# Optimization experiments

Measured on AMD Instinct MI355X. Metric: run time of the kernel, lower is better.

## Reference

```python
import jax, jax.numpy as jnp
import numpy as np

B = 131072
IN_DIM = 100
H = 256


def setup_inputs() -> dict:
    key = jax.random.key(0)
    ks = jax.random.split(key, 7)
    return {
        "x": jax.random.normal(ks[0], (B, IN_DIM), dtype=jnp.float32),
        "C": jax.random.normal(ks[1], (B, H), dtype=jnp.float32),
        "h": jax.random.normal(ks[2], (B, H), dtype=jnp.float32),
        # stacked gate weights, gate order: i, f, g, o  (equivalent to 8 separate Linears)
        "Wx": jax.random.normal(ks[3], (IN_DIM, 4 * H), dtype=jnp.float32) * 0.05,
        "Wh": jax.random.normal(ks[4], (H, 4 * H), dtype=jnp.float32) * 0.05,
        "bx": jax.random.normal(ks[5], (4 * H,), dtype=jnp.float32) * 0.05,
        "bh": jax.random.normal(ks[6], (4 * H,), dtype=jnp.float32) * 0.05,
    }


def reference(x, C, h, Wx, Wh, bx, bh):
    # two fused GEMMs replace the 8 per-gate Linears (same math)
    gates = (x @ Wx + bx) + (h @ Wh + bh)  # [B, 4H]
    i_pre, f_pre, g_pre, o_pre = jnp.split(gates, 4, axis=-1)
    i = jax.nn.sigmoid(i_pre)
    f = jax.nn.sigmoid(f_pre)
    g = jnp.tanh(g_pre)
    o = jax.nn.sigmoid(o_pre)
    c_out = f * C + i * g
    h_out = o * jnp.tanh(c_out)
    return (c_out, h_out)
```

## Files before the change

### kernel.cpp

```cpp
#include <hip/hip_runtime.h>
#include <stdint.h>


typedef short bf16x8 __attribute__((ext_vector_type(8)));
typedef float f32x4  __attribute__((ext_vector_type(4)));

#define HDIM   256
#define INDIM  100
#define NROWS  131072
#define BT_OFF 0
#define XB_OFF (1048576 / 2)
#define HB_OFF (35651584 / 2)
#define ABUF(b) ((b) * 8192)
#define BBUF(b) (24576 + (b) * 16384)

__device__ __forceinline__ float fexp(float x) {
  return __builtin_amdgcn_exp2f(x * 1.44269504088896340736f);
}
__device__ __forceinline__ float frcp(float x) { return __builtin_amdgcn_rcpf(x); }
__device__ __forceinline__ float sigm(float x) { return frcp(1.0f + fexp(-x)); }
__device__ __forceinline__ float tanh_fast(float x) {
  return 1.0f - 2.0f * frcp(1.0f + fexp(2.0f * x));
}
__device__ __forceinline__ unsigned short f2bf_rne(float f) {
  union { float f; uint32_t u; } v; v.f = f;
  return (unsigned short)((v.u + 0x7FFFu + ((v.u >> 16) & 1u)) >> 16);
}
__device__ __forceinline__ void gl16(const void* g, void* l) {
  __builtin_amdgcn_global_load_lds(
      (const __attribute__((address_space(1))) unsigned int*)g,
      (__attribute__((address_space(3))) unsigned int*)l, 16, 0, 0);
}
#define VMW(N) asm volatile("s_waitcnt vmcnt(" #N ")" ::: "memory")

__global__ void prep_all(const float* __restrict__ X, const float* __restrict__ Hin,
                         const float* __restrict__ Wx, const float* __restrict__ Wh,
                         const float* __restrict__ bxp, const float* __restrict__ bhp,
                         unsigned short* __restrict__ ws) {
  const int b = blockIdx.x, tid = threadIdx.x;
  if (b < 8192) {
    const int t   = b * 256 + tid;
    const int row = t >> 4, k0 = (t & 15) * 8;
    const float* xp = X + (size_t)row * INDIM;
    float4 lo = make_float4(0.f, 0.f, 0.f, 0.f);
    float4 hi = make_float4(0.f, 0.f, 0.f, 0.f);
    if (k0 + 4 <= INDIM) lo = *reinterpret_cast<const float4*>(xp + k0);
    if (k0 + 8 <= INDIM) hi = *reinterpret_cast<const float4*>(xp + k0 + 4);
    float va[8] = {lo.x, lo.y, lo.z, lo.w, hi.x, hi.y, hi.z, hi.w};
    unsigned short o[8];
#pragma unroll
    for (int e = 0; e < 8; ++e) {
      const int k = k0 + e;
      const float f = (k < INDIM) ? va[e] : (k == 127 ? 1.0f : 0.0f);
      o[e] = f2bf_rne(f);
    }
    *reinterpret_cast<bf16x8*>(ws + XB_OFF + (size_t)row * 128 + k0) =
        *reinterpret_cast<bf16x8*>(o);
  } else if (b < 24576) {
    const int t   = (b - 8192) * 256 + tid;
    const int row = t >> 5, k0 = (t & 31) * 8;
    const float* hp = Hin + (size_t)row * HDIM + k0;
    const float4 lo = *reinterpret_cast<const float4*>(hp);
    const float4 hi = *reinterpret_cast<const float4*>(hp + 4);
    unsigned short o[8] = {f2bf_rne(lo.x), f2bf_rne(lo.y), f2bf_rne(lo.z),
                           f2bf_rne(lo.w), f2bf_rne(hi.x), f2bf_rne(hi.y),
                           f2bf_rne(hi.z), f2bf_rne(hi.w)};
    *reinterpret_cast<bf16x8*>(ws + HB_OFF + (size_t)row * 256 + k0) =
        *reinterpret_cast<bf16x8*>(o);
  } else {
    const int unit = (b - 24576) * 4 + (tid >> 6);
    const int lane = tid & 63;
    const int kst  = unit % 12;
    const int fidb = unit / 12;
    const int bn   = fidb >> 3, fid = fidb & 7;
    const int g    = fid >> 1,  wc  = fid & 1;
    const int wcol = g * HDIM + bn * 32 + wc * 16 + (lane & 15);
    const int kb   = kst * 32 + (lane >> 4) * 8;
    unsigned short v[8];
#pragma unroll
    for (int e = 0; e < 8; ++e) {
      const int k = kb + e;
      float f = 0.0f;
      if (k < INDIM)     f = Wx[(size_t)k * 1024 + wcol];
      else if (k == 127) f = bxp[wcol] + bhp[wcol];
      else if (k >= 128) f = Wh[(size_t)(k - 128) * 1024 + wcol];
      v[e] = f2bf_rne(f);
    }
    *reinterpret_cast<bf16x8*>(ws + BT_OFF + (size_t)unit * 512 + lane * 8) =
        *reinterpret_cast<bf16x8*>(v);
  }
}

__global__ __launch_bounds__(512, 2)
void lstm_main(const unsigned short* __restrict__ ws,
               const float* __restrict__ Cin, float* __restrict__ out)
{
  __shared__ unsigned char smem[73728];

  const int tid  = threadIdx.x;
  const int orig = blockIdx.x;
  const int lg   = ((orig & 7) << 9) | (orig >> 3);
  const int mt   = lg >> 2;
  const int bnn  = lg & 3;

  const int lane = tid & 63;
  const int l15  = lane & 15;
  const int kq   = lane >> 4;
  const int wid  = tid >> 6;
  const int wr   = wid >> 2;
  const int wcq  = wid & 3;
  const int ch   = bnn * 64 + wcq * 16 + l15;
  const int sx   = (l15 >> 1) & 3;

  const unsigned short* xb = ws + XB_OFF;
  const unsigned short* hb = ws + HB_OFF;
  const unsigned short* Bt = ws + BT_OFF;

  const int ci = wid * 64 + lane;
  const int r  = ci >> 2;
  const int sc = (ci & 3) ^ ((r >> 1) & 3);
  const unsigned short* xsrc = xb + (size_t)(mt * 128 + r) * 128 + sc * 8;
  const unsigned short* hsrc = hb + (size_t)(mt * 128 + r) * 256 + sc * 8;

  const unsigned short* bsrc[2];
#pragma unroll
  for (int j = 0; j < 2; ++j) {
    const int u  = wid * 2 + j;
    const int gu = (bnn * 2 + (u >> 3)) * 8 + (u & 7);
    bsrc[j] = Bt + (size_t)gu * 12 * 512 + lane * 8;
  }
  const int adst = wid * 1024;
  const int bd0  = (wid * 2 + 0) * 1024;
  const int bd1  = (wid * 2 + 1) * 1024;

  f32x4 acc[4][4];
#pragma unroll
  for (int m = 0; m < 4; ++m)
#pragma unroll
    for (int g = 0; g < 4; ++g)
#pragma unroll
      for (int e = 0; e < 4; ++e) acc[m][g][e] = 0.0f;

  float cvv[4][4];

  auto STAGE = [&](int T) {
    char* Ad = (char*)smem + ABUF(T % 3);
    char* Bd = (char*)smem + BBUF(T % 3);
    if (T < 4) gl16(xsrc + T * 32, Ad + adst);
    else       gl16(hsrc + (T - 4) * 32, Ad + adst);
    gl16(bsrc[0] + T * 512, Bd + bd0);
    gl16(bsrc[1] + T * 512, Bd + bd1);
  };

  auto COMPUTE = [&](int S) {
    const unsigned short* Ab = (const unsigned short*)(smem + ABUF(S % 3));
    const unsigned short* Bb = (const unsigned short*)(smem + BBUF(S % 3));
    bf16x8 afr[4], bfr[4];
#pragma unroll
    for (int m = 0; m < 4; ++m)
      afr[m] = *reinterpret_cast<const bf16x8*>(
          Ab + (wr * 64 + m * 16 + l15) * 32 + ((kq ^ sx) * 8));
#pragma unroll
    for (int g = 0; g < 4; ++g) {
      const int ub = (wcq >> 1) * 8 + g * 2 + (wcq & 1);
      bfr[g] = *reinterpret_cast<const bf16x8*>(Bb + ub * 512 + lane * 8);
    }
    __builtin_amdgcn_s_setprio(1);
#pragma unroll
    for (int m = 0; m < 4; ++m)
#pragma unroll
      for (int g = 0; g < 4; ++g)
        acc[m][g] = __builtin_amdgcn_mfma_f32_16x16x32_bf16(
            afr[m], bfr[g], acc[m][g], 0, 0, 0);
    __builtin_amdgcn_s_setprio(0);
  };

  STAGE(0);
  STAGE(1);

#define STEP(S, KN)                                               \
  do {                                                            \
    VMW(KN);                                                      \
    __builtin_amdgcn_s_barrier();                                 \
    if ((S) + 2 < 12) STAGE((S) + 2);                             \
    if ((S) == 9) {                                               \
      const float* cb =                                           \
          Cin + ((size_t)mt * 128 + wr * 64 + kq * 4) * HDIM + ch;\
      _Pragma("unroll")                                           \
      for (int m = 0; m < 4; ++m)                                 \
        _Pragma("unroll")                                         \
        for (int e = 0; e < 4; ++e)                               \
          cvv[m][e] = __builtin_nontemporal_load(                 \
              cb + (size_t)(m * 16 + e) * HDIM);                  \
    }                                                             \
    COMPUTE(S);                                                   \
  } while (0)

  STEP(0, 3);  STEP(1, 3);  STEP(2, 3);  STEP(3, 3);
  STEP(4, 3);  STEP(5, 3);  STEP(6, 3);  STEP(7, 3);
  STEP(8, 3);  STEP(9, 3);  STEP(10, 19); STEP(11, 16);
#undef STEP

  VMW(0);

  float* op  = out + ((size_t)mt * 128 + wr * 64 + kq * 4) * HDIM + ch;
  float* op2 = op + (size_t)NROWS * HDIM;
#pragma unroll
  for (int m = 0; m < 4; ++m) {
#pragma unroll
    for (int e = 0; e < 4; ++e) {
      const float pi = acc[m][0][e];
      const float pf = acc[m][1][e];
      const float pg = acc[m][2][e];
      const float po = acc[m][3][e];
      const float ig = sigm(pi), fg = sigm(pf);
      const float gg = tanh_fast(pg), og = sigm(po);
      const float co = fg * cvv[m][e] + ig * gg;
      const float ho = og * tanh_fast(co);
      __builtin_nontemporal_store(co, op  + (size_t)(m * 16 + e) * HDIM);
      __builtin_nontemporal_store(ho, op2 + (size_t)(m * 16 + e) * HDIM);
    }
  }
}

extern "C" void kernel_launch(void* const* d_in, const int* in_sizes, int n_in,
                              void* d_out, int out_size, void* d_ws, size_t ws_size,
                              hipStream_t stream) {
  const float* x  = (const float*)d_in[0];
  const float* C  = (const float*)d_in[1];
  const float* h  = (const float*)d_in[2];
  const float* Wx = (const float*)d_in[3];
  const float* Wh = (const float*)d_in[4];
  const float* bx = (const float*)d_in[5];
  const float* bh = (const float*)d_in[6];
  float* o = (float*)d_out;
  unsigned short* ws = (unsigned short*)d_ws;

  prep_all<<<dim3(24768), dim3(256), 0, stream>>>(x, h, Wx, Wh, bx, bh, ws);
  lstm_main<<<dim3(4096), dim3(512), 0, stream>>>(ws, C, o);
}
```

Baseline: 195.6 us.

## Load B weight fragments directly from global into registers, bypassing LDS

Weight (B) tiles are no longer staged through shared memory via global_load_lds. Each wave now loads its four bf16x8 B fragments straight into double-buffered registers, two stages ahead, and the vmcnt wait counts are adjusted to match. This shrinks LDS per block from 72KB to 24KB and removes the LDS writes and reads for B, which could allow more resident blocks. In exchange, weights that several waves used to share through LDS are now fetched redundantly from global/L2, and register pressure rises.

```diff
diff --git a/kernel.cpp b/kernel.cpp
--- a/kernel.cpp
+++ b/kernel.cpp
@@ -12,7 +12,6 @@
 #define XB_OFF (1048576 / 2)
 #define HB_OFF (35651584 / 2)
 #define ABUF(b) ((b) * 8192)
-#define BBUF(b) (24576 + (b) * 16384)
 
 __device__ __forceinline__ float fexp(float x) {
   return __builtin_amdgcn_exp2f(x * 1.44269504088896340736f);
@@ -95,7 +94,7 @@
 void lstm_main(const unsigned short* __restrict__ ws,
                const float* __restrict__ Cin, float* __restrict__ out)
 {
-  __shared__ unsigned char smem[73728];
+  __shared__ unsigned char smem[24576];
 
   const int tid  = threadIdx.x;
   const int orig = blockIdx.x;
@@ -121,17 +120,15 @@
   const int sc = (ci & 3) ^ ((r >> 1) & 3);
   const unsigned short* xsrc = xb + (size_t)(mt * 128 + r) * 128 + sc * 8;
   const unsigned short* hsrc = hb + (size_t)(mt * 128 + r) * 256 + sc * 8;
-
-  const unsigned short* bsrc[2];
-#pragma unroll
-  for (int j = 0; j < 2; ++j) {
-    const int u  = wid * 2 + j;
-    const int gu = (bnn * 2 + (u >> 3)) * 8 + (u & 7);
-    bsrc[j] = Bt + (size_t)gu * 12 * 512 + lane * 8;
+  const int adst = wid * 1024;
+
+  const unsigned short* btp[4];
+#pragma unroll
+  for (int g = 0; g < 4; ++g) {
+    const int ub = (wcq >> 1) * 8 + g * 2 + (wcq & 1);
+    const int gu = (bnn * 2 + (ub >> 3)) * 8 + (ub & 7);
+    btp[g] = Bt + (size_t)gu * 12 * 512 + lane * 8;
   }
-  const int adst = wid * 1024;
-  const int bd0  = (wid * 2 + 0) * 1024;
-  const int bd1  = (wid * 2 + 1) * 1024;
 
   f32x4 acc[4][4];
 #pragma unroll
@@ -141,48 +138,46 @@
 #pragma unroll
       for (int e = 0; e < 4; ++e) acc[m][g][e] = 0.0f;
 
-  float cvv[4][4];
-
-  auto STAGE = [&](int T) {
+  float  cvv[4][4];
+  bf16x8 bfrA[4], bfrB[4];
+
+  auto STAGE_A = [&](int T) {
     char* Ad = (char*)smem + ABUF(T % 3);
-    char* Bd = (char*)smem + BBUF(T % 3);
     if (T < 4) gl16(xsrc + T * 32, Ad + adst);
     else       gl16(hsrc + (T - 4) * 32, Ad + adst);
-    gl16(bsrc[0] + T * 512, Bd + bd0);
-    gl16(bsrc[1] + T * 512, Bd + bd1);
   };
-
-  auto COMPUTE = [&](int S) {
+  auto LOADB = [&](int S, bf16x8 (&set)[4]) {
+#pragma unroll
+    for (int g = 0; g < 4; ++g)
+      set[g] = *reinterpret_cast<const bf16x8*>(btp[g] + S * 512);
+  };
+  auto COMPUTE = [&](int S, bf16x8 (&set)[4]) {
     const unsigned short* Ab = (const unsigned short*)(smem + ABUF(S % 3));
-    const unsigned short* Bb = (const unsigned short*)(smem + BBUF(S % 3));
-    bf16x8 afr[4], bfr[4];
+    bf16x8 afr[4];
 #pragma unroll
     for (int m = 0; m < 4; ++m)
       afr[m] = *reinterpret_cast<const bf16x8*>(
           Ab + (wr * 64 + m * 16 + l15) * 32 + ((kq ^ sx) * 8));
-#pragma unroll
-    for (int g = 0; g < 4; ++g) {
-      const int ub = (wcq >> 1) * 8 + g * 2 + (wcq & 1);
-      bfr[g] = *reinterpret_cast<const bf16x8*>(Bb + ub * 512 + lane * 8);
-    }
     __builtin_amdgcn_s_setprio(1);
 #pragma unroll
     for (int m = 0; m < 4; ++m)
 #pragma unroll
       for (int g = 0; g < 4; ++g)
         acc[m][g] = __builtin_amdgcn_mfma_f32_16x16x32_bf16(
-            afr[m], bfr[g], acc[m][g], 0, 0, 0);
+            afr[m], set[g], acc[m][g], 0, 0, 0);
     __builtin_amdgcn_s_setprio(0);
   };
 
-  STAGE(0);
-  STAGE(1);
-
-#define STEP(S, KN)                                               \
+  STAGE_A(0);  LOADB(0, bfrA);
+  STAGE_A(1);  LOADB(1, bfrB);
+
+#define STEP(S, KN, SET)                                          \
   do {                                                            \
     VMW(KN);                                                      \
     __builtin_amdgcn_s_barrier();                                 \
-    if ((S) + 2 < 12) STAGE((S) + 2);                             \
+    if ((S) + 2 < 12) STAGE_A((S) + 2);                           \
+    COMPUTE(S, SET);                                              \
+    if ((S) + 2 < 12) LOADB((S) + 2, SET);                        \
     if ((S) == 9) {                                               \
       const float* cb =                                           \
           Cin + ((size_t)mt * 128 + wr * 64 + kq * 4) * HDIM + ch;\
@@ -193,12 +188,11 @@
           cvv[m][e] = __builtin_nontemporal_load(                 \
               cb + (size_t)(m * 16 + e) * HDIM);                  \
     }                                                             \
-    COMPUTE(S);                                                   \
   } while (0)
 
-  STEP(0, 3);  STEP(1, 3);  STEP(2, 3);  STEP(3, 3);
-  STEP(4, 3);  STEP(5, 3);  STEP(6, 3);  STEP(7, 3);
-  STEP(8, 3);  STEP(9, 3);  STEP(10, 19); STEP(11, 16);
+  STEP(0, 5, bfrA);  STEP(1, 5, bfrB);  STEP(2, 5, bfrA);  STEP(3, 5, bfrB);
+  STEP(4, 5, bfrA);  STEP(5, 5, bfrB);  STEP(6, 5, bfrA);  STEP(7, 5, bfrB);
+  STEP(8, 5, bfrA);  STEP(9, 5, bfrB);  STEP(10, 21, bfrA); STEP(11, 16, bfrB);
 #undef STEP
 
   VMW(0);
```

Result: slower. 213.4 us (+9.1%).
